# Performance work log

Measured on AMD Instinct MI355X. Metric: run time of the kernel, lower is better.

## Reference

```python
import jax, jax.numpy as jnp
import numpy as np

B, S, H = 2, 2048, 2048
NH = 16
HD = H // NH  # 128


def setup_inputs() -> dict:
    key = jax.random.key(0)
    ks = jax.random.split(key, 6)
    sc = 0.02
    return {
        "x": jax.random.normal(ks[0], (B, S, H), dtype=jnp.float32),
        "attention_mask": jnp.zeros((B, S), dtype=jnp.float32),
        "Wq": jax.random.normal(ks[1], (H, H), dtype=jnp.float32) * sc,
        "bq": jnp.zeros((H,), dtype=jnp.float32),
        "Wk": jax.random.normal(ks[2], (H, H), dtype=jnp.float32) * sc,
        "bk": jnp.zeros((H,), dtype=jnp.float32),
        "Wv": jax.random.normal(ks[3], (H, H), dtype=jnp.float32) * sc,
        "bv": jnp.zeros((H,), dtype=jnp.float32),
        "Wo": jax.random.normal(ks[4], (H, H), dtype=jnp.float32) * sc,
        "bo": jnp.zeros((H,), dtype=jnp.float32),
    }


def reference(x, attention_mask, Wq, bq, Wk, bk, Wv, bv, Wo, bo):
    b, s, h = x.shape
    q = (x @ Wq + bq).reshape(b, s, NH, HD)
    k = (x @ Wk + bk).reshape(b, s, NH, HD)
    v = (x @ Wv + bv).reshape(b, s, NH, HD)
    scale = 1.0 / jnp.sqrt(jnp.asarray(HD, dtype=x.dtype))
    scores = jnp.einsum('bqhd,bkhd->bhqk', q, k) * scale
    scores = scores + attention_mask[:, None, None, :]
    weights = jax.nn.softmax(scores, axis=-1)
    attn = jnp.einsum('bhqk,bkhd->bqhd', weights, v).reshape(b, s, h)
    return attn @ Wo + bo
```

## Files before the change

kernel.cpp:

```cpp
#include <hip/hip_runtime.h>
#include <hip/hip_bf16.h>
#include <stdint.h>

#define BB   2
#define SS   2048
#define HHH  2048
#define NHH  16
#define HDD  128
#define MTOT 4096

typedef __bf16 bf16x8 __attribute__((ext_vector_type(8)));
typedef float  f32x4  __attribute__((ext_vector_type(4)));
typedef float  f32x16 __attribute__((ext_vector_type(16)));

#define MFMA16(a, b, c) __builtin_amdgcn_mfma_f32_16x16x32_bf16((a), (b), (c), 0, 0, 0)
#define MFMA32(a, b, c) __builtin_amdgcn_mfma_f32_32x32x16_bf16((a), (b), (c), 0, 0, 0)

__device__ __forceinline__ unsigned short f2bf(float f) {
    union { float f; unsigned u; } v; v.f = f;
    unsigned r = v.u + 0x7FFFu + ((v.u >> 16) & 1u);
    return (unsigned short)(r >> 16);
}

__device__ __forceinline__ unsigned packbf(float a, float b) {
    union { __bf16 h[2]; unsigned u; } p;
    p.h[0] = (__bf16)a; p.h[1] = (__bf16)b;
    return p.u;
}

__device__ __forceinline__ void pswap(unsigned &a, unsigned &b) {
    asm("v_permlane32_swap_b32 %0, %1" : "+v"(a), "+v"(b));
}

__device__ __forceinline__ float2 xswap(float x) {
    unsigned a = __builtin_bit_cast(unsigned, x);
    unsigned b;
    asm("v_mov_b32 %0, %1" : "=v"(b) : "v"(a));
    asm("v_permlane32_swap_b32 %0, %1" : "+v"(a), "+v"(b));
    return make_float2(__builtin_bit_cast(float, a), __builtin_bit_cast(float, b));
}

__device__ __forceinline__ void gload16(const void* src, void* lds) {
    __builtin_amdgcn_global_load_lds(
        (__attribute__((address_space(1))) void*)src,
        (__attribute__((address_space(3))) void*)lds,
        16, 0, 0);
}

__global__ void prep_all(const float* __restrict__ x, unsigned short* __restrict__ xb,
                         const float* __restrict__ mask, float* __restrict__ mkl,
                         const float* __restrict__ W0, const float* __restrict__ W1,
                         const float* __restrict__ W2, const float* __restrict__ W3,
                         unsigned short* __restrict__ Wt) {
    __shared__ float tile[32][33];
    int bid = blockIdx.x;
    if (bid < 16384) {
        int z = bid >> 12, rem = bid & 4095;
        int bx = rem & 63, by = rem >> 6;
        const float* in = z == 0 ? W0 : z == 1 ? W1 : z == 2 ? W2 : W3;
        unsigned short* o = Wt + (size_t)z * ((size_t)HHH * HHH);
        int c0 = bx * 32, r0 = by * 32;
        int tx = threadIdx.x & 31, ty = threadIdx.x >> 5;
        #pragma unroll
        for (int i = 0; i < 32; i += 8)
            tile[ty + i][tx] = in[(size_t)(r0 + ty + i) * HHH + c0 + tx];
        __syncthreads();
        #pragma unroll
        for (int i = 0; i < 32; i += 8)
            o[(size_t)(c0 + ty + i) * HHH + r0 + tx] = f2bf(tile[tx][ty + i]);
        return;
    }
    bid -= 16384;
    if (bid >= 2048) {
        int i = (bid - 2048) * 256 + threadIdx.x;
        mkl[i] = mask[i] * 1.4426950408889634f;
        return;
    }
    const int n = MTOT * HHH;
    const int stride = 2048 * 256 * 4;
    for (int i = (bid * 256 + threadIdx.x) * 4; i < n; i += stride) {
        float4 v = *(const float4*)(x + i);
        ushort4 o;
        o.x = f2bf(v.x); o.y = f2bf(v.y); o.z = f2bf(v.z); o.w = f2bf(v.w);
        *(ushort4*)(xb + i) = o;
    }
}

__global__ __launch_bounds__(512, 2) void gemmQK(
    const unsigned short* __restrict__ A,
    const unsigned short* __restrict__ Bt,
    const float* __restrict__ bq,
    const float* __restrict__ bk,
    unsigned short* __restrict__ Qb,
    unsigned short* __restrict__ Kb)
{
    __shared__ __align__(16) unsigned char sm[131072];
    const int tid = threadIdx.x;
    const int wv = tid >> 6, ln = tid & 63;
    const int g = ln >> 4, r = ln & 15;
    const int wr = wv >> 2, wc = wv & 3;
    const int K = HHH;

    const int bid = blockIdx.x;
    const int xc = bid & 7, j = bid >> 3;
    const int m0 = ((xc >> 1) * 4 + (j & 3)) * 256;
    const int n0 = ((xc & 1) * 8 + (j >> 2)) * 256;

    unsigned srcA[4], srcB[4];
    int ldsA[4], ldsB[4];
    #pragma unroll
    for (int jj = 0; jj < 4; ++jj) {
        int o = jj * 8192 + tid * 16;
        int row = o >> 7;
        int lg = ((o >> 4) & 7) ^ (row & 7);
        srcA[jj] = (unsigned)(m0 + row) * K + lg * 8;
        srcB[jj] = (unsigned)(n0 + row) * K + lg * 8;
        ldsA[jj] = o;
        ldsB[jj] = 32768 + o;
    }

    f32x4 acc[8][4];
    #pragma unroll
    for (int i = 0; i < 8; ++i)
        #pragma unroll
        for (int jj = 0; jj < 4; ++jj)
            acc[i][jj] = (f32x4){0.f, 0.f, 0.f, 0.f};

    #pragma unroll
    for (int jj = 0; jj < 4; ++jj) { gload16(A + srcA[jj], sm + ldsA[jj]);
                                     gload16(Bt + srcB[jj], sm + ldsB[jj]); }
    #pragma unroll
    for (int jj = 0; jj < 4; ++jj) { gload16(A + srcA[jj] + 64, sm + 65536 + ldsA[jj]);
                                     gload16(Bt + srcB[jj] + 64, sm + 65536 + ldsB[jj]); }
    asm volatile("s_waitcnt vmcnt(8)" ::: "memory");
    __builtin_amdgcn_s_barrier();

    #define LDA(mi, ks) (*(const bf16x8*)(Ab + (wr * 128 + (mi) * 16 + r) * 128 + \
                         ((((ks) << 2) + g) ^ ((wr * 128 + (mi) * 16 + r) & 7)) * 16))
    #define LDB(ni, ks) (*(const bf16x8*)(Bb + (wc * 64 + (ni) * 16 + r) * 128 + \
                         ((((ks) << 2) + g) ^ ((wc * 64 + (ni) * 16 + r) & 7)) * 16))

    for (int t = 0; t < 32; ++t) {
        const int base = (t & 1) * 65536;
        const unsigned char* Ab = sm + base;
        const unsigned char* Bb = Ab + 32768;
        unsigned char* Pb = sm + base;
        const bool pre = (t + 2 < 32);
        const int ko = (t + 2) * 64;

        bf16x8 af[4][2], bfr[2][2];

        #pragma unroll
        for (int mi = 0; mi < 4; ++mi) { af[mi][0] = LDA(mi, 0); af[mi][1] = LDA(mi, 1); }
        bfr[0][0] = LDB(0, 0); bfr[0][1] = LDB(0, 1);
        bfr[1][0] = LDB(1, 0); bfr[1][1] = LDB(1, 1);
        __builtin_amdgcn_s_barrier();
        asm volatile("s_waitcnt lgkmcnt(0)" ::: "memory");
        __builtin_amdgcn_s_setprio(1);
        #pragma unroll
        for (int mi = 0; mi < 4; ++mi)
            #pragma unroll
            for (int ni = 0; ni < 2; ++ni)
                #pragma unroll
                for (int ks = 0; ks < 2; ++ks)
                    acc[mi][ni] = MFMA16(af[mi][ks], bfr[ni][ks], acc[mi][ni]);
        __builtin_amdgcn_s_setprio(0);
        __builtin_amdgcn_s_barrier();

        bfr[0][0] = LDB(2, 0); bfr[0][1] = LDB(2, 1);
        bfr[1][0] = LDB(3, 0); bfr[1][1] = LDB(3, 1);
        __builtin_amdgcn_s_barrier();
        asm volatile("s_waitcnt lgkmcnt(0)" ::: "memory");
        __builtin_amdgcn_s_setprio(1);
        #pragma unroll
        for (int mi = 0; mi < 4; ++mi)
            #pragma unroll
            for (int ni = 0; ni < 2; ++ni)
                #pragma unroll
                for (int ks = 0; ks < 2; ++ks)
                    acc[mi][ni + 2] = MFMA16(af[mi][ks], bfr[ni][ks], acc[mi][ni + 2]);
        __builtin_amdgcn_s_setprio(0);
        __builtin_amdgcn_s_barrier();

        #pragma unroll
        for (int mi = 0; mi < 4; ++mi) { af[mi][0] = LDA(mi + 4, 0); af[mi][1] = LDA(mi + 4, 1); }
        if (pre) { gload16(A + srcA[0] + ko, Pb + ldsA[0]);
                   gload16(A + srcA[1] + ko, Pb + ldsA[1]); }
        __builtin_amdgcn_s_barrier();
        asm volatile("s_waitcnt lgkmcnt(0)" ::: "memory");
        __builtin_amdgcn_s_setprio(1);
        #pragma unroll
        for (int mi = 0; mi < 4; ++mi)
            #pragma unroll
            for (int ni = 0; ni < 2; ++ni)
                #pragma unroll
                for (int ks = 0; ks < 2; ++ks)
                    acc[mi + 4][ni + 2] = MFMA16(af[mi][ks], bfr[ni][ks], acc[mi + 4][ni + 2]);
        __builtin_amdgcn_s_setprio(0);
        __builtin_amdgcn_s_barrier();

        bfr[0][0] = LDB(0, 0); bfr[0][1] = LDB(0, 1);
        bfr[1][0] = LDB(1, 0); bfr[1][1] = LDB(1, 1);
        if (pre) { gload16(A + srcA[2] + ko, Pb + ldsA[2]);
                   gload16(A + srcA[3] + ko, Pb + ldsA[3]); }
        __builtin_amdgcn_s_barrier();
        asm volatile("s_waitcnt lgkmcnt(0)" ::: "memory");
        __builtin_amdgcn_s_setprio(1);
        #pragma unroll
        for (int mi = 0; mi < 4; ++mi)
            #pragma unroll
            for (int ni = 0; ni < 2; ++ni)
                #pragma unroll
                for (int ks = 0; ks < 2; ++ks)
                    acc[mi + 4][ni] = MFMA16(af[mi][ks], bfr[ni][ks], acc[mi + 4][ni]);
        __builtin_amdgcn_s_setprio(0);
        __builtin_amdgcn_s_barrier();

        if (pre) {
            #pragma unroll
            for (int jj = 0; jj < 4; ++jj)
                gload16(Bt + srcB[jj] + ko, Pb + ldsB[jj]);
            asm volatile("s_waitcnt vmcnt(8)" ::: "memory");
        } else {
            asm volatile("s_waitcnt vmcnt(0)" ::: "memory");
        }
        __builtin_amdgcn_s_barrier();
    }
    #undef LDA
    #undef LDB

    const int region = n0 >> 11;
    const float* bp = region ? bk : bq;
    unsigned short* outp = region ? Kb : Qb;
    #pragma unroll
    for (int mt = 0; mt < 8; ++mt) {
        #pragma unroll
        for (int nt = 0; nt < 4; ++nt) {
            int col = n0 + wc * 64 + nt * 16 + r;
            int lcol = col & 2047;
            float bvv = bp[lcol];
            f32x4 a = acc[mt][nt];
            int mrow = m0 + wr * 128 + mt * 16 + g * 4;
            #pragma unroll
            for (int q = 0; q < 4; ++q)
                outp[(size_t)(mrow + q) * 2048 + lcol] = f2bf(a[q] + bvv);
        }
    }
}

template<int MODE>
__global__ __launch_bounds__(512, 2) void gemm8_bf16(
    const unsigned short* __restrict__ A,
    const unsigned short* __restrict__ Bt,
    const float* __restrict__ bias,
    void* __restrict__ Cout,
    int M, int N, int K)
{
    __shared__ __align__(16) unsigned char sm[147456];
    const int tid = threadIdx.x;
    const int wv = tid >> 6, ln = tid & 63;
    const int g = ln >> 4, r = ln & 15;
    const int wr = wv >> 2, wc = wv & 3;

    const int bid = blockIdx.x;
    const int xc = bid & 7, j = bid >> 3;
    const int m0 = ((xc & 3) * 8 + (j & 7)) * 128;
    const int n0 = ((xc >> 2) * 4 + (j >> 3)) * 256;

    unsigned srcA[2]; int ldsA[2];
    #pragma unroll
    for (int jj = 0; jj < 2; ++jj) {
        int o = jj * 8192 + tid * 16;
        int row = o >> 7;
        int lg = ((o >> 4) & 7) ^ (row & 7);
        srcA[jj] = (unsigned)(m0 + row) * K + lg * 8;
        ldsA[jj] = o;
    }
    unsigned srcB[4]; int ldsB[4];
    #pragma unroll
    for (int jj = 0; jj < 4; ++jj) {
        int o = jj * 8192 + tid * 16;
        int row = o >> 7;
        int lg = ((o >> 4) & 7) ^ (row & 7);
        srcB[jj] = (unsigned)(n0 + row) * K + lg * 8;
        ldsB[jj] = 16384 + o;
    }

    f32x4 acc[4][4];
    #pragma unroll
    for (int i = 0; i < 4; ++i)
        #pragma unroll
        for (int jj = 0; jj < 4; ++jj)
            acc[i][jj] = (f32x4){0.f, 0.f, 0.f, 0.f};

    const int NT = K >> 6;

    {
        unsigned char* b0 = sm;
        unsigned char* b1 = sm + 49152;
        #pragma unroll
        for (int jj = 0; jj < 2; ++jj) gload16(A + srcA[jj], b0 + ldsA[jj]);
        #pragma unroll
        for (int jj = 0; jj < 4; ++jj) gload16(Bt + srcB[jj], b0 + ldsB[jj]);
        #pragma unroll
        for (int jj = 0; jj < 2; ++jj) gload16(A + srcA[jj] + 64, b1 + ldsA[jj]);
        #pragma unroll
        for (int jj = 0; jj < 4; ++jj) gload16(Bt + srcB[jj] + 64, b1 + ldsB[jj]);
    }
    asm volatile("s_waitcnt vmcnt(6)" ::: "memory");
    __builtin_amdgcn_s_barrier();

    #define LDA(mi, ks) (*(const bf16x8*)(Ab + (wr * 64 + (mi) * 16 + r) * 128 + \
                         ((((ks) << 2) + g) ^ ((wr * 64 + (mi) * 16 + r) & 7)) * 16))
    #define LDB(ni, ks) (*(const bf16x8*)(Bb + (wc * 64 + (ni) * 16 + r) * 128 + \
                         ((((ks) << 2) + g) ^ ((wc * 64 + (ni) * 16 + r) & 7)) * 16))

    int csel = 0, psel = 2;
    for (int t = 0; t < NT; ++t) {
        const unsigned char* Ab = sm + csel * 49152;
        const unsigned char* Bb = Ab + 16384;
        unsigned char* Pb = sm + psel * 49152;
        const bool pre = (t + 2 < NT);
        const int ko = (t + 2) * 64;

        bf16x8 af[2][2], bfr[4][2];

        af[0][0] = LDA(0, 0); af[0][1] = LDA(0, 1);
        af[1][0] = LDA(1, 0); af[1][1] = LDA(1, 1);
        #pragma unroll
        for (int ni = 0; ni < 4; ++ni) { bfr[ni][0] = LDB(ni, 0); bfr[ni][1] = LDB(ni, 1); }
        if (pre) { gload16(Bt + srcB[0] + ko, Pb + ldsB[0]);
                   gload16(Bt + srcB[1] + ko, Pb + ldsB[1]);
                   gload16(Bt + srcB[2] + ko, Pb + ldsB[2]); }
        __builtin_amdgcn_s_barrier();
        asm volatile("s_waitcnt lgkmcnt(0)" ::: "memory");
        __builtin_amdgcn_s_setprio(1);
        #pragma unroll
        for (int mi = 0; mi < 2; ++mi)
            #pragma unroll
            for (int ni = 0; ni < 4; ++ni)
                #pragma unroll
                for (int ks = 0; ks < 2; ++ks)
                    acc[mi][ni] = MFMA16(af[mi][ks], bfr[ni][ks], acc[mi][ni]);
        __builtin_amdgcn_s_setprio(0);
        __builtin_amdgcn_s_barrier();

        af[0][0] = LDA(2, 0); af[0][1] = LDA(2, 1);
        af[1][0] = LDA(3, 0); af[1][1] = LDA(3, 1);
        if (pre) { gload16(Bt + srcB[3] + ko, Pb + ldsB[3]);
                   gload16(A + srcA[0] + ko, Pb + ldsA[0]);
                   gload16(A + srcA[1] + ko, Pb + ldsA[1]); }
        __builtin_amdgcn_s_barrier();
        asm volatile("s_waitcnt lgkmcnt(0)" ::: "memory");
        __builtin_amdgcn_s_setprio(1);
        #pragma unroll
        for (int mi = 0; mi < 2; ++mi)
            #pragma unroll
            for (int ni = 0; ni < 4; ++ni)
                #pragma unroll
                for (int ks = 0; ks < 2; ++ks)
                    acc[mi + 2][ni] = MFMA16(af[mi][ks], bfr[ni][ks], acc[mi + 2][ni]);
        __builtin_amdgcn_s_setprio(0);

        if (pre) asm volatile("s_waitcnt vmcnt(6)" ::: "memory");
        else     asm volatile("s_waitcnt vmcnt(0)" ::: "memory");
        __builtin_amdgcn_s_barrier();

        csel = (csel == 2) ? 0 : csel + 1;
        psel = (psel == 2) ? 0 : psel + 1;
    }
    #undef LDA
    #undef LDB

    #pragma unroll
    for (int mt = 0; mt < 4; ++mt) {
        #pragma unroll
        for (int nt = 0; nt < 4; ++nt) {
            int col = n0 + wc * 64 + nt * 16 + r;
            float bvv = bias[col];
            f32x4 a = acc[mt][nt];
            int mrow = m0 + wr * 64 + mt * 16 + g * 4;
            if (MODE == 0) {
                #pragma unroll
                for (int q = 0; q < 4; ++q)
                    ((unsigned short*)Cout)[(size_t)(mrow + q) * N + col] = f2bf(a[q] + bvv);
            } else if (MODE == 2) {
                #pragma unroll
                for (int q = 0; q < 4; ++q)
                    ((float*)Cout)[(size_t)(mrow + q) * N + col] = a[q] + bvv;
            } else {
                int b = mrow >> 11, s0x = mrow & 2047;
                ushort4 o;
                o.x = f2bf(a[0] + bvv); o.y = f2bf(a[1] + bvv);
                o.z = f2bf(a[2] + bvv); o.w = f2bf(a[3] + bvv);
                *(ushort4*)((unsigned short*)Cout + ((size_t)(b * 2048 + col)) * 2048 + s0x) = o;
            }
        }
    }
}

__global__ __launch_bounds__(256, 2) void attn_fwd(
    const unsigned short* __restrict__ Q,
    const unsigned short* __restrict__ K,
    const unsigned short* __restrict__ V,
    const float* __restrict__ maskl2,
    unsigned short* __restrict__ O)
{
    __shared__ __align__(16) unsigned char sm[73728];
    const int tid = threadIdx.x, wv = tid >> 6, ln = tid & 63;
    const int hi = ln >> 5, qr = ln & 31;

    const int bid = blockIdx.x;
    const int lb = (bid & 7) * 64 + (bid >> 3);
    const int qb = lb & 15;
    const int bh = lb >> 4;
    const int h = bh & 15, b = bh >> 4;

    const size_t rowQ0 = (size_t)(b * 2048 + qb * 128 + wv * 32);
    const float SCL2 = 0.08838834764831845f * 1.4426950408889634f;

    unsigned srcK[4], srcV[4];
    int ldsK[4], ldsV[4];
    #pragma unroll
    for (int i = 0; i < 4; ++i) {
        int ch = wv * 4 + i;
        int o = ch * 1024 + ln * 16;
        { int row = o >> 8; int gl = ((o >> 4) & 15) ^ (row & 7);
          srcK[i] = (unsigned)((b * 2048 + row) * 2048 + h * 128 + gl * 8);
          ldsK[i] = o; }
        { int d = o >> 7; int gl = ((o >> 4) & 7) ^ (d & 7);
          srcV[i] = (unsigned)((b * 2048 + h * 128 + d) * 2048 + gl * 8);
          ldsV[i] = 16384 + o; }
    }

    #define STAGE(t, base) { \
        _Pragma("unroll") \
        for (int i = 0; i < 4; ++i) { \
            gload16(K + srcK[i] + (unsigned)(t) * (64u * 2048u), sm + (base) + ldsK[i]); \
            gload16(V + srcV[i] + (unsigned)(t) * 64u, sm + (base) + ldsV[i]); \
        } }

    #pragma unroll
    for (int i = 0; i < 2; ++i)
        gload16(maskl2 + b * 2048 + wv * 512 + i * 256 + ln * 4,
                sm + 65536 + wv * 2048 + i * 1024);
    STAGE(0, 0); STAGE(1, 32768);

    bf16x8 qf[8];
    #pragma unroll
    for (int ks = 0; ks < 8; ++ks)
        qf[ks] = *(const bf16x8*)(Q + (rowQ0 + qr) * 2048 + h * 128 + ks * 16 + hi * 8);

    f32x16 acc[4];
    #pragma unroll
    for (int i = 0; i < 4; ++i)
        #pragma unroll
        for (int jj = 0; jj < 16; ++jj)
            acc[i][jj] = 0.f;
    float mr = -3.0e38f, lr = 0.f;

    const float* ml = (const float*)(sm + 65536);

    asm volatile("s_waitcnt vmcnt(8)" ::: "memory");
    __builtin_amdgcn_s_barrier();

    for (int t = 0; t < 32; ++t) {
        const unsigned char* Kt = sm + (t & 1) * 32768;
        const unsigned char* Vt = Kt + 16384;

        f32x4 mk[2][4];
        #pragma unroll
        for (int kb2 = 0; kb2 < 2; ++kb2)
            #pragma unroll
            for (int rg = 0; rg < 4; ++rg)
                mk[kb2][rg] = *(const f32x4*)(ml + t * 64 + kb2 * 32 + rg * 8 + hi * 4);

        f32x16 sf0, sf1;
        #pragma unroll
        for (int jj = 0; jj < 16; ++jj) { sf0[jj] = 0.f; sf1[jj] = 0.f; }
        __builtin_amdgcn_s_setprio(1);
        #pragma unroll
        for (int ks = 0; ks < 8; ++ks) {
            int row0 = qr, row1 = 32 + qr;
            int s0 = ((2 * ks + hi) ^ (row0 & 7));
            int s1 = ((2 * ks + hi) ^ (row1 & 7));
            bf16x8 kf0 = *(const bf16x8*)(Kt + row0 * 256 + s0 * 16);
            bf16x8 kf1 = *(const bf16x8*)(Kt + row1 * 256 + s1 * 16);
            sf0 = MFMA32(kf0, qf[ks], sf0);
            sf1 = MFMA32(kf1, qf[ks], sf1);
        }
        __builtin_amdgcn_s_setprio(0);

        float sv[2][16];
        #pragma unroll
        for (int reg = 0; reg < 16; ++reg) {
            sv[0][reg] = sf0[reg] * SCL2 + mk[0][reg >> 2][reg & 3];
            sv[1][reg] = sf1[reg] * SCL2 + mk[1][reg >> 2][reg & 3];
        }

        float mx[8];
        #pragma unroll
        for (int jj = 0; jj < 8; ++jj)
            mx[jj] = fmaxf(fmaxf(sv[0][2*jj], sv[0][2*jj+1]),
                           fmaxf(sv[1][2*jj], sv[1][2*jj+1]));
        float m01 = fmaxf(fmaxf(fmaxf(mx[0], mx[1]), fmaxf(mx[2], mx[3])),
                          fmaxf(fmaxf(mx[4], mx[5]), fmaxf(mx[6], mx[7])));
        float2 mp = xswap(m01);
        float mt = fmaxf(mp.x, mp.y);

        float alpha = 1.f;
        int allskip = __all(mt <= mr + 8.f);
        if (!allskip) {
            float nm = fmaxf(mr, mt);
            alpha = __builtin_amdgcn_exp2f(mr - nm);
            mr = nm;
            #pragma unroll
            for (int dblk = 0; dblk < 4; ++dblk)
                #pragma unroll
                for (int reg = 0; reg < 16; ++reg)
                    acc[dblk][reg] *= alpha;
        }

        float s0 = 0.f, s1 = 0.f, s2 = 0.f, s3 = 0.f;
        #pragma unroll
        for (int kb2 = 0; kb2 < 2; ++kb2)
            #pragma unroll
            for (int reg = 0; reg < 16; reg += 4) {
                float p0 = __builtin_amdgcn_exp2f(sv[kb2][reg + 0] - mr);
                float p1 = __builtin_amdgcn_exp2f(sv[kb2][reg + 1] - mr);
                float p2 = __builtin_amdgcn_exp2f(sv[kb2][reg + 2] - mr);
                float p3 = __builtin_amdgcn_exp2f(sv[kb2][reg + 3] - mr);
                sv[kb2][reg + 0] = p0; sv[kb2][reg + 1] = p1;
                sv[kb2][reg + 2] = p2; sv[kb2][reg + 3] = p3;
                s0 += p0; s1 += p1; s2 += p2; s3 += p3;
            }
        float rsl = (s0 + s1) + (s2 + s3);
        float2 rp = xswap(rsl);
        float rs = rp.x + rp.y;
        lr = lr * alpha + rs;

        bf16x8 pfr[4];
        #pragma unroll
        for (int kb16 = 0; kb16 < 4; ++kb16) {
            const int kb2 = kb16 >> 1, i2 = kb16 & 1;
            float* pv = sv[kb2];
            unsigned W00 = packbf(pv[(2*i2+0)*4 + 0], pv[(2*i2+0)*4 + 1]);
            unsigned W01 = packbf(pv[(2*i2+0)*4 + 2], pv[(2*i2+0)*4 + 3]);
            unsigned W10 = packbf(pv[(2*i2+1)*4 + 0], pv[(2*i2+1)*4 + 1]);
            unsigned W11 = packbf(pv[(2*i2+1)*4 + 2], pv[(2*i2+1)*4 + 3]);
            pswap(W00, W10);
            pswap(W01, W11);
            union { unsigned w[4]; bf16x8 v; } u;
            u.w[0] = W00; u.w[1] = W01; u.w[2] = W10; u.w[3] = W11;
            pfr[kb16] = u.v;
        }

        __builtin_amdgcn_s_setprio(1);
        #pragma unroll
        for (int dblk = 0; dblk < 4; ++dblk) {
            int d = dblk * 32 + qr;
            f32x16 a = acc[dblk];
            #pragma unroll
            for (int kb16 = 0; kb16 < 4; ++kb16) {
                int s = ((2 * kb16 + hi) ^ (d & 7));
                bf16x8 vf = *(const bf16x8*)(Vt + d * 128 + s * 16);
                a = MFMA32(vf, pfr[kb16], a);
            }
            acc[dblk] = a;
        }
        __builtin_amdgcn_s_setprio(0);

        __builtin_amdgcn_s_barrier();
        if (t + 2 < 32) {
            STAGE(t + 2, (t & 1) * 32768);
            asm volatile("s_waitcnt vmcnt(8)" ::: "memory");
        } else {
            asm volatile("s_waitcnt vmcnt(0)" ::: "memory");
        }
        __builtin_amdgcn_s_barrier();
    }

    float linv = 1.f / lr;
    unsigned short* orow = O + (rowQ0 + qr) * 2048 + h * 128;
    #pragma unroll
    for (int dblk = 0; dblk < 4; ++dblk)
        #pragma unroll
        for (int rg = 0; rg < 4; ++rg) {
            float v0 = acc[dblk][rg * 4 + 0] * linv;
            float v1 = acc[dblk][rg * 4 + 1] * linv;
            float v2 = acc[dblk][rg * 4 + 2] * linv;
            float v3 = acc[dblk][rg * 4 + 3] * linv;
            uint2 o;
            o.x = packbf(v0, v1);
            o.y = packbf(v2, v3);
            *(uint2*)(orow + dblk * 32 + rg * 8 + hi * 4) = o;
        }
    #undef STAGE
}

extern "C" void kernel_launch(void* const* d_in, const int* in_sizes, int n_in,
                              void* d_out, int out_size, void* d_ws, size_t ws_size,
                              hipStream_t stream)
{
    (void)in_sizes; (void)n_in; (void)out_size; (void)ws_size;
    const float* x    = (const float*)d_in[0];
    const float* mask = (const float*)d_in[1];
    const float* Wq   = (const float*)d_in[2];
    const float* bq   = (const float*)d_in[3];
    const float* Wk   = (const float*)d_in[4];
    const float* bk   = (const float*)d_in[5];
    const float* Wv   = (const float*)d_in[6];
    const float* bv   = (const float*)d_in[7];
    const float* Wo   = (const float*)d_in[8];
    const float* bo   = (const float*)d_in[9];
    float* out = (float*)d_out;

    char* ws = (char*)d_ws;
    unsigned short* xb  = (unsigned short*)(ws);
    unsigned short* Wqt = (unsigned short*)(ws + (16u << 20));
    unsigned short* Wvt = (unsigned short*)(ws + (32u << 20));
    unsigned short* Wot = (unsigned short*)(ws + (40u << 20));
    unsigned short* Qb  = (unsigned short*)(ws + (48u << 20));
    unsigned short* Kb  = (unsigned short*)(ws + (64u << 20));
    unsigned short* Vtb = (unsigned short*)(ws + (80u << 20));
    unsigned short* Ab  = (unsigned short*)(ws + (16u << 20));
    float*          mkl = out;

    prep_all<<<18436, 256, 0, stream>>>(x, xb, mask, mkl, Wq, Wk, Wv, Wo, Wqt);

    gemmQK<<<256, 512, 0, stream>>>(xb, Wqt, bq, bk, Qb, Kb);
    gemm8_bf16<1><<<256, 512, 0, stream>>>(xb, Wvt, bv, Vtb, MTOT, HHH, HHH);

    attn_fwd<<<512, 256, 0, stream>>>(Qb, Kb, Vtb, mkl, Ab);

    gemm8_bf16<2><<<256, 512, 0, stream>>>(Ab, Wot, bo, out, MTOT, HHH, HHH);
}
```

Measured before the change: 257.1 us.

## Retile attention to 16x16 MFMA with 64-row query blocks and 32-key tiles

Rewrites the attention kernel to use 16x16x32 MFMA, giving each wave 16 query rows. The key tile shrinks to 32, which cuts LDS to 40KB and raises launch bounds to 3 blocks per CU, and the grid doubles to 1024 blocks. The aim is higher occupancy and more parallelism. In exchange each K/V tile is reused by fewer query rows, so global and LDS traffic rises, and each iteration does more softmax reduction through the extra permlane16 swaps, plus more barriers.

```diff
diff --git a/kernel.cpp b/kernel.cpp
--- a/kernel.cpp
+++ b/kernel.cpp
@@ -14,7 +14,6 @@
 typedef float  f32x16 __attribute__((ext_vector_type(16)));
 
 #define MFMA16(a, b, c) __builtin_amdgcn_mfma_f32_16x16x32_bf16((a), (b), (c), 0, 0, 0)
-#define MFMA32(a, b, c) __builtin_amdgcn_mfma_f32_32x32x16_bf16((a), (b), (c), 0, 0, 0)
 
 __device__ __forceinline__ unsigned short f2bf(float f) {
     union { float f; unsigned u; } v; v.f = f;
@@ -28,15 +27,25 @@
     return p.u;
 }
 
-__device__ __forceinline__ void pswap(unsigned &a, unsigned &b) {
+__device__ __forceinline__ void pswap32(unsigned &a, unsigned &b) {
     asm("v_permlane32_swap_b32 %0, %1" : "+v"(a), "+v"(b));
 }
-
-__device__ __forceinline__ float2 xswap(float x) {
+__device__ __forceinline__ void pswap16(unsigned &a, unsigned &b) {
+    asm("v_permlane16_swap_b32 %0, %1" : "+v"(a), "+v"(b));
+}
+
+__device__ __forceinline__ float2 xswap32(float x) {
     unsigned a = __builtin_bit_cast(unsigned, x);
     unsigned b;
     asm("v_mov_b32 %0, %1" : "=v"(b) : "v"(a));
     asm("v_permlane32_swap_b32 %0, %1" : "+v"(a), "+v"(b));
+    return make_float2(__builtin_bit_cast(float, a), __builtin_bit_cast(float, b));
+}
+__device__ __forceinline__ float2 xswap16(float x) {
+    unsigned a = __builtin_bit_cast(unsigned, x);
+    unsigned b;
+    asm("v_mov_b32 %0, %1" : "=v"(b) : "v"(a));
+    asm("v_permlane16_swap_b32 %0, %1" : "+v"(a), "+v"(b));
     return make_float2(__builtin_bit_cast(float, a), __builtin_bit_cast(float, b));
 }
 
@@ -399,114 +408,102 @@
     }
 }
 
-__global__ __launch_bounds__(256, 2) void attn_fwd(
+__global__ __launch_bounds__(256, 3) void attn_fwd(
     const unsigned short* __restrict__ Q,
     const unsigned short* __restrict__ K,
     const unsigned short* __restrict__ V,
     const float* __restrict__ maskl2,
     unsigned short* __restrict__ O)
 {
-    __shared__ __align__(16) unsigned char sm[73728];
+    __shared__ __align__(16) unsigned char sm[40960];
     const int tid = threadIdx.x, wv = tid >> 6, ln = tid & 63;
-    const int hi = ln >> 5, qr = ln & 31;
+    const int g = ln >> 4, q16 = ln & 15;
 
     const int bid = blockIdx.x;
-    const int lb = (bid & 7) * 64 + (bid >> 3);
-    const int qb = lb & 15;
-    const int bh = lb >> 4;
+    const int lb = (bid & 7) * 128 + (bid >> 3);
+    const int qb = lb & 31;
+    const int bh = lb >> 5;
     const int h = bh & 15, b = bh >> 4;
 
-    const size_t rowQ0 = (size_t)(b * 2048 + qb * 128 + wv * 32);
+    const size_t rowQ0 = (size_t)(b * 2048 + qb * 64 + wv * 16);
     const float SCL2 = 0.08838834764831845f * 1.4426950408889634f;
 
-    unsigned srcK[4], srcV[4];
-    int ldsK[4], ldsV[4];
-    #pragma unroll
-    for (int i = 0; i < 4; ++i) {
-        int ch = wv * 4 + i;
+    bf16x8 qf[4];
+    #pragma unroll
+    for (int ks = 0; ks < 4; ++ks)
+        qf[ks] = *(const bf16x8*)(Q + (rowQ0 + q16) * 2048 + h * 128 + ks * 32 + g * 8);
+
+    unsigned srcK[2], srcV[2];
+    int ldsK[2], ldsV[2];
+    #pragma unroll
+    for (int i = 0; i < 2; ++i) {
+        int ch = wv * 2 + i;
         int o = ch * 1024 + ln * 16;
         { int row = o >> 8; int gl = ((o >> 4) & 15) ^ (row & 7);
           srcK[i] = (unsigned)((b * 2048 + row) * 2048 + h * 128 + gl * 8);
           ldsK[i] = o; }
-        { int d = o >> 7; int gl = ((o >> 4) & 7) ^ (d & 7);
+        { int d = o >> 6; int gl = ((o >> 4) & 3) ^ ((d >> 1) & 3);
           srcV[i] = (unsigned)((b * 2048 + h * 128 + d) * 2048 + gl * 8);
-          ldsV[i] = 16384 + o; }
+          ldsV[i] = 8192 + o; }
     }
 
     #define STAGE(t, base) { \
         _Pragma("unroll") \
-        for (int i = 0; i < 4; ++i) { \
-            gload16(K + srcK[i] + (unsigned)(t) * (64u * 2048u), sm + (base) + ldsK[i]); \
-            gload16(V + srcV[i] + (unsigned)(t) * 64u, sm + (base) + ldsV[i]); \
+        for (int i = 0; i < 2; ++i) { \
+            gload16(K + srcK[i] + (unsigned)(t) * (32u * 2048u), sm + (base) + ldsK[i]); \
+            gload16(V + srcV[i] + (unsigned)(t) * 32u, sm + (base) + ldsV[i]); \
         } }
 
     #pragma unroll
-    for (int i = 0; i < 2; ++i)
-        gload16(maskl2 + b * 2048 + wv * 512 + i * 256 + ln * 4,
-                sm + 65536 + wv * 2048 + i * 1024);
-    STAGE(0, 0); STAGE(1, 32768);
-
-    bf16x8 qf[8];
-    #pragma unroll
-    for (int ks = 0; ks < 8; ++ks)
-        qf[ks] = *(const bf16x8*)(Q + (rowQ0 + qr) * 2048 + h * 128 + ks * 16 + hi * 8);
-
-    f32x16 acc[4];
-    #pragma unroll
-    for (int i = 0; i < 4; ++i)
-        #pragma unroll
-        for (int jj = 0; jj < 16; ++jj)
-            acc[i][jj] = 0.f;
+    for (int it = 0; it < 2; ++it)
+        gload16(maskl2 + b * 2048 + it * 1024 + wv * 256 + ln * 4,
+                sm + 32768 + it * 4096 + wv * 1024 + ln * 16);
+    STAGE(0, 0); STAGE(1, 16384);
+
+    f32x4 acc[8];
+    #pragma unroll
+    for (int i = 0; i < 8; ++i)
+        acc[i] = (f32x4){0.f, 0.f, 0.f, 0.f};
     float mr = -3.0e38f, lr = 0.f;
 
-    const float* ml = (const float*)(sm + 65536);
-
-    asm volatile("s_waitcnt vmcnt(8)" ::: "memory");
+    const float* ml = (const float*)(sm + 32768);
+
+    asm volatile("s_waitcnt vmcnt(4)" ::: "memory");
     __builtin_amdgcn_s_barrier();
 
-    for (int t = 0; t < 32; ++t) {
-        const unsigned char* Kt = sm + (t & 1) * 32768;
-        const unsigned char* Vt = Kt + 16384;
-
-        f32x4 mk[2][4];
-        #pragma unroll
-        for (int kb2 = 0; kb2 < 2; ++kb2)
-            #pragma unroll
-            for (int rg = 0; rg < 4; ++rg)
-                mk[kb2][rg] = *(const f32x4*)(ml + t * 64 + kb2 * 32 + rg * 8 + hi * 4);
-
-        f32x16 sf0, sf1;
-        #pragma unroll
-        for (int jj = 0; jj < 16; ++jj) { sf0[jj] = 0.f; sf1[jj] = 0.f; }
-        __builtin_amdgcn_s_setprio(1);
-        #pragma unroll
-        for (int ks = 0; ks < 8; ++ks) {
-            int row0 = qr, row1 = 32 + qr;
-            int s0 = ((2 * ks + hi) ^ (row0 & 7));
-            int s1 = ((2 * ks + hi) ^ (row1 & 7));
+    for (int t = 0; t < 64; ++t) {
+        const unsigned char* Kt = sm + (t & 1) * 16384;
+        const unsigned char* Vt = Kt + 8192;
+
+        f32x4 mk0 = *(const f32x4*)(ml + t * 32 + 4 * g);
+        f32x4 mk1 = *(const f32x4*)(ml + t * 32 + 16 + 4 * g);
+
+        f32x4 S0 = (f32x4){0.f,0.f,0.f,0.f}, S1 = S0;
+        __builtin_amdgcn_s_setprio(1);
+        #pragma unroll
+        for (int ks = 0; ks < 4; ++ks) {
+            int row0 = q16, row1 = 16 + q16;
+            int s0 = (ks * 4 + g) ^ (q16 & 7);
             bf16x8 kf0 = *(const bf16x8*)(Kt + row0 * 256 + s0 * 16);
-            bf16x8 kf1 = *(const bf16x8*)(Kt + row1 * 256 + s1 * 16);
-            sf0 = MFMA32(kf0, qf[ks], sf0);
-            sf1 = MFMA32(kf1, qf[ks], sf1);
-        }
-        __builtin_amdgcn_s_setprio(0);
-
-        float sv[2][16];
-        #pragma unroll
-        for (int reg = 0; reg < 16; ++reg) {
-            sv[0][reg] = sf0[reg] * SCL2 + mk[0][reg >> 2][reg & 3];
-            sv[1][reg] = sf1[reg] * SCL2 + mk[1][reg >> 2][reg & 3];
-        }
-
-        float mx[8];
-        #pragma unroll
-        for (int jj = 0; jj < 8; ++jj)
-            mx[jj] = fmaxf(fmaxf(sv[0][2*jj], sv[0][2*jj+1]),
-                           fmaxf(sv[1][2*jj], sv[1][2*jj+1]));
-        float m01 = fmaxf(fmaxf(fmaxf(mx[0], mx[1]), fmaxf(mx[2], mx[3])),
-                          fmaxf(fmaxf(mx[4], mx[5]), fmaxf(mx[6], mx[7])));
-        float2 mp = xswap(m01);
-        float mt = fmaxf(mp.x, mp.y);
+            bf16x8 kf1 = *(const bf16x8*)(Kt + row1 * 256 + s0 * 16);
+            S0 = MFMA16(kf0, qf[ks], S0);
+            S1 = MFMA16(kf1, qf[ks], S1);
+        }
+        __builtin_amdgcn_s_setprio(0);
+
+        float sv[8];
+        #pragma unroll
+        for (int r2 = 0; r2 < 4; ++r2) {
+            sv[r2]     = S0[r2] * SCL2 + mk0[r2];
+            sv[4 + r2] = S1[r2] * SCL2 + mk1[r2];
+        }
+
+        float m01 = fmaxf(fmaxf(fmaxf(sv[0], sv[1]), fmaxf(sv[2], sv[3])),
+                          fmaxf(fmaxf(sv[4], sv[5]), fmaxf(sv[6], sv[7])));
+        float2 p16 = xswap16(m01);
+        float m2 = fmaxf(p16.x, p16.y);
+        float2 p32 = xswap32(m2);
+        float mt = fmaxf(p32.x, p32.y);
 
         float alpha = 1.f;
         int allskip = __all(mt <= mr + 8.f);
@@ -515,87 +512,64 @@
             alpha = __builtin_amdgcn_exp2f(mr - nm);
             mr = nm;
             #pragma unroll
-            for (int dblk = 0; dblk < 4; ++dblk)
-                #pragma unroll
-                for (int reg = 0; reg < 16; ++reg)
-                    acc[dblk][reg] *= alpha;
-        }
-
-        float s0 = 0.f, s1 = 0.f, s2 = 0.f, s3 = 0.f;
-        #pragma unroll
-        for (int kb2 = 0; kb2 < 2; ++kb2)
-            #pragma unroll
-            for (int reg = 0; reg < 16; reg += 4) {
-                float p0 = __builtin_amdgcn_exp2f(sv[kb2][reg + 0] - mr);
-                float p1 = __builtin_amdgcn_exp2f(sv[kb2][reg + 1] - mr);
-                float p2 = __builtin_amdgcn_exp2f(sv[kb2][reg + 2] - mr);
-                float p3 = __builtin_amdgcn_exp2f(sv[kb2][reg + 3] - mr);
-                sv[kb2][reg + 0] = p0; sv[kb2][reg + 1] = p1;
-                sv[kb2][reg + 2] = p2; sv[kb2][reg + 3] = p3;
-                s0 += p0; s1 += p1; s2 += p2; s3 += p3;
-            }
-        float rsl = (s0 + s1) + (s2 + s3);
-        float2 rp = xswap(rsl);
-        float rs = rp.x + rp.y;
+            for (int dblk = 0; dblk < 8; ++dblk)
+                #pragma unroll
+                for (int r2 = 0; r2 < 4; ++r2)
+                    acc[dblk][r2] *= alpha;
+        }
+
+        float s0 = 0.f;
+        #pragma unroll
+        for (int r2 = 0; r2 < 8; ++r2) {
+            float p = __builtin_amdgcn_exp2f(sv[r2] - mr);
+            sv[r2] = p;
+            s0 += p;
+        }
+        float2 s16 = xswap16(s0);
+        float s2 = s16.x + s16.y;
+        float2 s32 = xswap32(s2);
+        float rs = s32.x + s32.y;
         lr = lr * alpha + rs;
 
-        bf16x8 pfr[4];
-        #pragma unroll
-        for (int kb16 = 0; kb16 < 4; ++kb16) {
-            const int kb2 = kb16 >> 1, i2 = kb16 & 1;
-            float* pv = sv[kb2];
-            unsigned W00 = packbf(pv[(2*i2+0)*4 + 0], pv[(2*i2+0)*4 + 1]);
-            unsigned W01 = packbf(pv[(2*i2+0)*4 + 2], pv[(2*i2+0)*4 + 3]);
-            unsigned W10 = packbf(pv[(2*i2+1)*4 + 0], pv[(2*i2+1)*4 + 1]);
-            unsigned W11 = packbf(pv[(2*i2+1)*4 + 2], pv[(2*i2+1)*4 + 3]);
-            pswap(W00, W10);
-            pswap(W01, W11);
-            union { unsigned w[4]; bf16x8 v; } u;
-            u.w[0] = W00; u.w[1] = W01; u.w[2] = W10; u.w[3] = W11;
-            pfr[kb16] = u.v;
-        }
-
-        __builtin_amdgcn_s_setprio(1);
-        #pragma unroll
-        for (int dblk = 0; dblk < 4; ++dblk) {
-            int d = dblk * 32 + qr;
-            f32x16 a = acc[dblk];
-            #pragma unroll
-            for (int kb16 = 0; kb16 < 4; ++kb16) {
-                int s = ((2 * kb16 + hi) ^ (d & 7));
-                bf16x8 vf = *(const bf16x8*)(Vt + d * 128 + s * 16);
-                a = MFMA32(vf, pfr[kb16], a);
-            }
-            acc[dblk] = a;
-        }
-        __builtin_amdgcn_s_setprio(0);
-
-        __builtin_amdgcn_s_barrier();
-        if (t + 2 < 32) {
-            STAGE(t + 2, (t & 1) * 32768);
-            asm volatile("s_waitcnt vmcnt(8)" ::: "memory");
+        unsigned w0 = packbf(sv[0], sv[1]);
+        unsigned w1 = packbf(sv[2], sv[3]);
+        unsigned w2 = packbf(sv[4], sv[5]);
+        unsigned w3 = packbf(sv[6], sv[7]);
+        pswap32(w0, w2); pswap16(w0, w2);
+        pswap32(w1, w3); pswap16(w1, w3);
+        union { unsigned w[4]; bf16x8 v; } pu;
+        pu.w[0] = w0; pu.w[1] = w1; pu.w[2] = w2; pu.w[3] = w3;
+
+        __builtin_amdgcn_s_setprio(1);
+        #pragma unroll
+        for (int dblk = 0; dblk < 8; ++dblk) {
+            int d = dblk * 16 + q16;
+            int s = g ^ ((d >> 1) & 3);
+            bf16x8 vf = *(const bf16x8*)(Vt + d * 64 + s * 16);
+            acc[dblk] = MFMA16(vf, pu.v, acc[dblk]);
+        }
+        __builtin_amdgcn_s_setprio(0);
+
+        __builtin_amdgcn_s_barrier();
+        if (t + 2 < 64) {
+            STAGE(t + 2, (t & 1) * 16384);
+            asm volatile("s_waitcnt vmcnt(4)" ::: "memory");
         } else {
             asm volatile("s_waitcnt vmcnt(0)" ::: "memory");
         }
         __builtin_amdgcn_s_barrier();
     }
+    #undef STAGE
 
     float linv = 1.f / lr;
-    unsigned short* orow = O + (rowQ0 + qr) * 2048 + h * 128;
-    #pragma unroll
-    for (int dblk = 0; dblk < 4; ++dblk)
-        #pragma unroll
-        for (int rg = 0; rg < 4; ++rg) {
-            float v0 = acc[dblk][rg * 4 + 0] * linv;
-            float v1 = acc[dblk][rg * 4 + 1] * linv;
-            float v2 = acc[dblk][rg * 4 + 2] * linv;
-            float v3 = acc[dblk][rg * 4 + 3] * linv;
-            uint2 o;
-            o.x = packbf(v0, v1);
-            o.y = packbf(v2, v3);
-            *(uint2*)(orow + dblk * 32 + rg * 8 + hi * 4) = o;
-        }
-    #undef STAGE
+    unsigned short* orow = O + (rowQ0 + q16) * 2048 + h * 128;
+    #pragma unroll
+    for (int dblk = 0; dblk < 8; ++dblk) {
+        uint2 o;
+        o.x = packbf(acc[dblk][0] * linv, acc[dblk][1] * linv);
+        o.y = packbf(acc[dblk][2] * linv, acc[dblk][3] * linv);
+        *(uint2*)(orow + dblk * 16 + 4 * g) = o;
+    }
 }
 
 extern "C" void kernel_launch(void* const* d_in, const int* in_sizes, int n_in,
@@ -631,7 +605,7 @@
     gemmQK<<<256, 512, 0, stream>>>(xb, Wqt, bq, bk, Qb, Kb);
     gemm8_bf16<1><<<256, 512, 0, stream>>>(xb, Wvt, bv, Vtb, MTOT, HHH, HHH);
 
-    attn_fwd<<<512, 256, 0, stream>>>(Qb, Kb, Vtb, mkl, Ab);
+    attn_fwd<<<1024, 256, 0, stream>>>(Qb, Kb, Vtb, mkl, Ab);
 
     gemm8_bf16<2><<<256, 512, 0, stream>>>(Ab, Wot, bo, out, MTOT, HHH, HHH);
 }
```

Result: slower. 270.6 us (+5.3%).
